# Kernel optimization log

Hardware: AMD Instinct MI355X
Metric: run time of the kernel (lower is better)

## Reference

```python
import jax, jax.numpy as jnp
import numpy as np
import math

TWO_PI = 2.0 * math.pi
LN_EPS = 1e-5


def _phase(pos_f, d):
    # periods[i, j] = i * d + j + 2 ; phi[s, i, j] = cos(2*pi*k_s / periods[i, j])
    i = jnp.arange(d, dtype=jnp.float32)
    periods = i[:, None] * d + i[None, :] + 2.0  # (d, d)
    return jnp.cos(TWO_PI * pos_f[:, None, None] / periods)  # (S, d, d)


def _layernorm(x, g, b):
    mu = jnp.mean(x, axis=-1, keepdims=True)
    var = jnp.mean(jnp.square(x - mu), axis=-1, keepdims=True)
    return (x - mu) * jax.lax.rsqrt(var + LN_EPS) * g + b


def _pos_nk(x, P, phi):
    # Nk[b, s, i] = sum_j P[i, j] * x[b, s, j] * phi[s, i, j]
    return jnp.einsum('bsj,ij,sij->bsi', x, P, phi)


def setup_inputs() -> dict:
    key = jax.random.key(0)
    ks = jax.random.split(key, 10)
    B, S, V, D = 4, 4096, 64, 128
    NTOK = 64  # 4^3 k-mer tokens
    u = lambda k, shp, a: jax.random.uniform(k, shp, jnp.float32, -a, a)
    return {
        'tokens': jax.random.randint(ks[0], (B, S), 0, NTOK, dtype=jnp.int32),
        'positions': jnp.arange(S, dtype=jnp.int32),
        'emb': jax.random.normal(ks[1], (NTOK, V), jnp.float32),
        'char_P': u(ks[2], (V, V), 0.1),
        'M1': u(ks[3], (D, V), 0.5),
        'P1': u(ks[4], (D, D), 0.1),
        'g1': jnp.ones((D,), jnp.float32),
        'b1': jnp.zeros((D,), jnp.float32),
        'R1': u(ks[5], (D, V), 0.1),
        'M2': u(ks[6], (D, D), 0.5),
        'P2': u(ks[7], (D, D), 0.1),
        'g2': jnp.ones((D,), jnp.float32),
        'b2': jnp.zeros((D,), jnp.float32),
    }


def reference(tokens, positions, emb, char_P, M1, P1, g1, b1, R1, M2, P2, g2, b2):
    pos_f = positions.astype(jnp.float32)
    V, D1, D2 = emb.shape[1], M1.shape[0], M2.shape[0]
    # char level (Layer 0): embedding + position-modulated mixing
    x = emb[tokens]                               # (B, S, V)
    h = _pos_nk(x, char_P, _phase(pos_f, V))      # (B, S, V)
    # Layer 1: separate residual (in_dim != out_dim -> linear proj)
    t1 = jnp.einsum('bsj,ij->bsi', h, M1)         # (B, S, D1)
    n1 = _pos_nk(_layernorm(t1, g1, b1), P1, _phase(pos_f, D1))
    h1 = n1 + jnp.einsum('bsj,ij->bsi', h, R1)
    # Layer 2: shared residual (residual = x @ M.T, pre-norm)
    t2 = jnp.einsum('bsj,ij->bsi', h1, M2)        # (B, S, D2)
    n2 = _pos_nk(_layernorm(t2, g2, b2), P2, _phase(pos_f, D2))
    return n2 + t2
```

## Files before the change

kernel.cpp:

```cpp
#include <hip/hip_runtime.h>

typedef unsigned short u16;
typedef unsigned int   u32;

#define BB 4
#define SS 4096
#define VV 64
#define DD 128

#define CPT_OFF 0
#define M1T_OFF 4096
#define R1T_OFF 12288
#define P1T_OFF 20480
#define M2T_OFF 36864
#define P2T_OFF 53248
#define EMB_OFF 69632
#define G1_OFF  73728
#define B1_OFF  73856
#define G2_OFF  73984
#define B2_OFF  74112
#define WS_F32_WEIGHTS 74240

__device__ __forceinline__ float bf2f(u16 u) {
    return __uint_as_float(((u32)u) << 16);
}
__device__ __forceinline__ float ldany(const void* p, int idx, bool f32) {
    return f32 ? ((const float*)p)[idx] : bf2f(((const u16*)p)[idx]);
}
__device__ __forceinline__ float phase_cos(float pos, float pf) {
    float x = pos * __builtin_amdgcn_rcpf(pf);
    float r = x - floorf(x);
    return __builtin_amdgcn_cosf(r);
}
__device__ __forceinline__ u32 pk_bf16(float lo, float hi) {
    u32 a = __float_as_uint(lo) + 0x8000u;
    u32 b = __float_as_uint(hi) + 0x8000u;
    return __builtin_amdgcn_perm(b, a, 0x07060302u);
}
__device__ __forceinline__ float bfhalf(u32 word, int hi) {
    return __uint_as_float(hi ? (word & 0xffff0000u) : (word << 16));
}
__device__ __forceinline__ float f4get(float4 v, int i) {
    return i == 0 ? v.x : i == 1 ? v.y : i == 2 ? v.z : v.w;
}
__device__ __forceinline__ float4 f4sum(float4 a, float4 b) {
    return make_float4(a.x + b.x, a.y + b.y, a.z + b.z, a.w + b.w);
}
__device__ __forceinline__ float4 fma4(float s, float4 v, float4 a) {
    return make_float4(fmaf(s, v.x, a.x), fmaf(s, v.y, a.y),
                       fmaf(s, v.z, a.z), fmaf(s, v.w, a.w));
}

__global__ void prep_ws(const void* __restrict__ cP,  const void* __restrict__ M1,
                        const void* __restrict__ R1,  const void* __restrict__ P1,
                        const void* __restrict__ M2,  const void* __restrict__ P2,
                        const void* __restrict__ emb, const void* __restrict__ g1,
                        const void* __restrict__ b1,  const void* __restrict__ g2,
                        const void* __restrict__ b2,  float* __restrict__ wsf)
{
    const bool f32 = (((const u32*)g1)[0] == 0x3F800000u);
    const int m = blockIdx.x;
    const int t = threadIdx.x;
    if (m == 17) {
        for (int idx = t; idx < 4608; idx += 256) {
            float v; int dst;
            if (idx < 4096) { v = ldany(emb, idx, f32); dst = EMB_OFF + idx; }
            else {
                int off = idx - 4096, which = off >> 7, e = off & 127;
                const void* p = (which == 0) ? g1 : (which == 1) ? b1
                              : (which == 2) ? g2 : b2;
                v = ldany(p, e, f32);
                dst = G1_OFF + which * 128 + e;
            }
            wsf[dst] = v;
        }
        return;
    }
    __shared__ float tile[64][65];
    const void* src; int doff, R, C, ti0, tj0;
    if (m == 0)      { src = cP; doff = CPT_OFF; R = 64;  C = 64;  ti0 = 0;            tj0 = 0; }
    else if (m <= 2) { src = M1; doff = M1T_OFF; R = 128; C = 64;  ti0 = (m - 1) * 64; tj0 = 0; }
    else if (m <= 4) { src = R1; doff = R1T_OFF; R = 128; C = 64;  ti0 = (m - 3) * 64; tj0 = 0; }
    else {
        const int k = m - 5, w = k >> 2, q = k & 3;
        src  = (w == 0) ? P1 : (w == 1) ? M2 : P2;
        doff = (w == 0) ? P1T_OFF : (w == 1) ? M2T_OFF : P2T_OFF;
        R = 128; C = 128; ti0 = (q >> 1) * 64; tj0 = (q & 1) * 64;
    }
    float* dst = wsf + doff;
    #pragma unroll
    for (int k = 0; k < 16; ++k) {
        int idx = k * 256 + t;
        int i = idx >> 6, j = idx & 63;
        tile[i][j] = ldany(src, (ti0 + i) * C + (tj0 + j), f32);
    }
    __syncthreads();
    #pragma unroll
    for (int k = 0; k < 16; ++k) {
        int idx = k * 256 + t;
        int j = idx >> 6, i = idx & 63;
        int gj = tj0 + j, gi = ti0 + i;
        dst[((gj >> 2) * R + gi) * 4 + (gj & 3)] = tile[i][j];
    }
}

template<bool WS>
__global__ void __launch_bounds__(256, 4)
fused_hier(const int* __restrict__ tokens,
           const int* __restrict__ positions,
           const void* __restrict__ emb,
           const void* __restrict__ cP,
           const void* __restrict__ M1,
           const void* __restrict__ P1,
           const void* __restrict__ g1,
           const void* __restrict__ b1,
           const void* __restrict__ R1,
           const void* __restrict__ M2,
           const void* __restrict__ P2,
           const void* __restrict__ g2,
           const void* __restrict__ b2,
           const float* __restrict__ wsf,
           float* __restrict__ out)
{
    __shared__ float4 x4v[VV];
    __shared__ float4 h4v[VV];
    __shared__ float4 lnv[DD];
    __shared__ float4 h1v[DD];
    __shared__ float4 t2v[DD];
    __shared__ float4 t14v[DD];
    __shared__ float4 partv[512];

    float* lnf = (float*)lnv;

    const int t = threadIdx.x;
    const int s = blockIdx.x;
    if (s >= SS) return;
    const bool f32 = WS ? true : (((const u32*)g1)[0] == 0x3F800000u);
    const float pos = (float)positions[s];
    const int i6 = t & 63,  q4 = t >> 6;
    const int i7 = t & 127, h2 = t >> 7;
    const int w  = t >> 6,  l  = t & 63;

    if (t < 64) {
        int tk0 = tokens[0 * SS + s], tk1 = tokens[1 * SS + s];
        int tk2 = tokens[2 * SS + s], tk3 = tokens[3 * SS + s];
        float4 xb;
        xb.x = WS ? wsf[EMB_OFF + tk0 * VV + i6] : ldany(emb, tk0 * VV + i6, f32);
        xb.y = WS ? wsf[EMB_OFF + tk1 * VV + i6] : ldany(emb, tk1 * VV + i6, f32);
        xb.z = WS ? wsf[EMB_OFF + tk2 * VV + i6] : ldany(emb, tk2 * VV + i6, f32);
        xb.w = WS ? wsf[EMB_OFF + tk3 * VV + i6] : ldany(emb, tk3 * VV + i6, f32);
        x4v[i6] = xb;
    }
    __syncthreads();

    {
        float4 a = make_float4(0, 0, 0, 0);
        const int jb = q4 * 16;
        float pf = (float)(i6 * VV + jb + 2);
        #pragma unroll
        for (int q = 0; q < 4; ++q) {
            const int jg = q4 * 4 + q;
            float4 w4;
            if (WS) w4 = *(const float4*)&wsf[CPT_OFF + (jg * VV + i6) * 4];
            #pragma unroll
            for (int k = 0; k < 4; ++k) {
                const int j = jb + q * 4 + k;
                float c  = phase_cos(pos, pf);
                float wt = (WS ? f4get(w4, k) : ldany(cP, i6 * VV + j, f32)) * c;
                a = fma4(wt, x4v[j], a);
                pf += 1.0f;
            }
        }
        partv[q4 * 64 + i6] = a;
    }
    __syncthreads();

    if (t < 64) {
        h4v[i6] = f4sum(f4sum(partv[i6], partv[64 + i6]),
                        f4sum(partv[128 + i6], partv[192 + i6]));
    }
    __syncthreads();

    {
        float4 at = make_float4(0, 0, 0, 0), ar = make_float4(0, 0, 0, 0);
        #pragma unroll
        for (int q = 0; q < 8; ++q) {
            const int jg = h2 * 8 + q;
            float4 m4, r4;
            if (WS) {
                m4 = *(const float4*)&wsf[M1T_OFF + (jg * DD + i7) * 4];
                r4 = *(const float4*)&wsf[R1T_OFF + (jg * DD + i7) * 4];
            }
            #pragma unroll
            for (int k = 0; k < 4; ++k) {
                const int j = h2 * 32 + q * 4 + k;
                float mv = WS ? f4get(m4, k) : ldany(M1, i7 * VV + j, f32);
                float rv = WS ? f4get(r4, k) : ldany(R1, i7 * VV + j, f32);
                float4 hb = h4v[j];
                at = fma4(mv, hb, at);
                ar = fma4(rv, hb, ar);
            }
        }
        partv[h2 * 128 + i7]       = at;
        partv[256 + h2 * 128 + i7] = ar;
    }
    __syncthreads();

    if (t < 128) {
        t14v[i7] = f4sum(partv[i7], partv[128 + i7]);
        h1v[i7]  = f4sum(partv[256 + i7], partv[384 + i7]);
    }
    __syncthreads();

    {
        float v0 = f4get(t14v[l], w), v1 = f4get(t14v[l + 64], w);
        float s1 = v0 + v1;
        #pragma unroll
        for (int m = 1; m < 64; m <<= 1) s1 += __shfl_xor(s1, m, 64);
        float mu = s1 * (1.0f / 128.0f);
        float d0 = v0 - mu, d1 = v1 - mu;
        float s2 = d0 * d0 + d1 * d1;
        #pragma unroll
        for (int m = 1; m < 64; m <<= 1) s2 += __shfl_xor(s2, m, 64);
        float rs = rsqrtf(s2 * (1.0f / 128.0f) + 1e-5f);
        float ga = WS ? wsf[G1_OFF + l]      : ldany(g1, l, f32);
        float gb = WS ? wsf[G1_OFF + l + 64] : ldany(g1, l + 64, f32);
        float ba = WS ? wsf[B1_OFF + l]      : ldany(b1, l, f32);
        float bb = WS ? wsf[B1_OFF + l + 64] : ldany(b1, l + 64, f32);
        lnf[l * 4 + w]        = d0 * rs * ga + ba;
        lnf[(l + 64) * 4 + w] = d1 * rs * gb + bb;
    }
    __syncthreads();

    u32 phc[32];
    {
        float4 acc = make_float4(0, 0, 0, 0);
        float pf = (float)(i7 * DD + h2 * 64 + 2);
        float cprev = 0.f;
        #pragma unroll
        for (int o = 0; o < 8; ++o) {
            float4 wa, wb;
            if (WS) {
                wa = *(const float4*)&wsf[P1T_OFF + ((h2 * 16 + 2 * o    ) * DD + i7) * 4];
                wb = *(const float4*)&wsf[P1T_OFF + ((h2 * 16 + 2 * o + 1) * DD + i7) * 4];
            }
            #pragma unroll
            for (int e = 0; e < 8; ++e) {
                const int j = h2 * 64 + o * 8 + e;
                float c = phase_cos(pos, pf);
                pf += 1.0f;
                if ((e & 1) == 0) cprev = c;
                else phc[o * 4 + (e >> 1)] = pk_bf16(cprev, c);
                float wv = WS ? (e < 4 ? f4get(wa, e) : f4get(wb, e - 4))
                              : ldany(P1, i7 * DD + j, f32);
                acc = fma4(wv * c, lnv[j], acc);
            }
        }
        partv[h2 * 128 + i7] = acc;
    }
    __syncthreads();

    if (t < 128) {
        h1v[i7] = f4sum(h1v[i7], f4sum(partv[i7], partv[128 + i7]));
    }
    __syncthreads();

    {
        float4 acc = make_float4(0, 0, 0, 0);
        #pragma unroll
        for (int q = 0; q < 16; ++q) {
            const int jg = h2 * 16 + q;
            float4 m4;
            if (WS) m4 = *(const float4*)&wsf[M2T_OFF + (jg * DD + i7) * 4];
            #pragma unroll
            for (int k = 0; k < 4; ++k) {
                const int j = h2 * 64 + q * 4 + k;
                float mv = WS ? f4get(m4, k) : ldany(M2, i7 * DD + j, f32);
                acc = fma4(mv, h1v[j], acc);
            }
        }
        partv[h2 * 128 + i7] = acc;
    }
    __syncthreads();

    if (t < 128) {
        t2v[i7] = f4sum(partv[i7], partv[128 + i7]);
    }
    __syncthreads();

    {
        float v0 = f4get(t2v[l], w), v1 = f4get(t2v[l + 64], w);
        float s1 = v0 + v1;
        #pragma unroll
        for (int m = 1; m < 64; m <<= 1) s1 += __shfl_xor(s1, m, 64);
        float mu = s1 * (1.0f / 128.0f);
        float d0 = v0 - mu, d1 = v1 - mu;
        float s2 = d0 * d0 + d1 * d1;
        #pragma unroll
        for (int m = 1; m < 64; m <<= 1) s2 += __shfl_xor(s2, m, 64);
        float rs = rsqrtf(s2 * (1.0f / 128.0f) + 1e-5f);
        float ga = WS ? wsf[G2_OFF + l]      : ldany(g2, l, f32);
        float gb = WS ? wsf[G2_OFF + l + 64] : ldany(g2, l + 64, f32);
        float ba = WS ? wsf[B2_OFF + l]      : ldany(b2, l, f32);
        float bb = WS ? wsf[B2_OFF + l + 64] : ldany(b2, l + 64, f32);
        lnf[l * 4 + w]        = d0 * rs * ga + ba;
        lnf[(l + 64) * 4 + w] = d1 * rs * gb + bb;
    }
    __syncthreads();

    {
        float4 acc = make_float4(0, 0, 0, 0);
        #pragma unroll
        for (int o = 0; o < 8; ++o) {
            float4 wa, wb;
            if (WS) {
                wa = *(const float4*)&wsf[P2T_OFF + ((h2 * 16 + 2 * o    ) * DD + i7) * 4];
                wb = *(const float4*)&wsf[P2T_OFF + ((h2 * 16 + 2 * o + 1) * DD + i7) * 4];
            }
            #pragma unroll
            for (int e = 0; e < 8; ++e) {
                const int j = h2 * 64 + o * 8 + e;
                float c = bfhalf(phc[o * 4 + (e >> 1)], e & 1);
                float wv = WS ? (e < 4 ? f4get(wa, e) : f4get(wb, e - 4))
                              : ldany(P2, i7 * DD + j, f32);
                acc = fma4(wv * c, lnv[j], acc);
            }
        }
        partv[h2 * 128 + i7] = acc;
    }
    __syncthreads();

    if (t < 128) {
        float4 n2 = f4sum(partv[i7], partv[128 + i7]);
        float4 o4 = f4sum(n2, t2v[i7]);
        out[(0 * SS + s) * DD + i7] = o4.x;
        out[(1 * SS + s) * DD + i7] = o4.y;
        out[(2 * SS + s) * DD + i7] = o4.z;
        out[(3 * SS + s) * DD + i7] = o4.w;
    }
}

extern "C" void kernel_launch(void* const* d_in, const int* in_sizes, int n_in,
                              void* d_out, int out_size, void* d_ws, size_t ws_size,
                              hipStream_t stream)
{
    const int* tokens    = (const int*)d_in[0];
    const int* positions = (const int*)d_in[1];
    const void* emb = d_in[2];
    const void* cP  = d_in[3];
    const void* M1  = d_in[4];
    const void* P1  = d_in[5];
    const void* g1  = d_in[6];
    const void* b1  = d_in[7];
    const void* R1  = d_in[8];
    const void* M2  = d_in[9];
    const void* P2  = d_in[10];
    const void* g2  = d_in[11];
    const void* b2  = d_in[12];
    float* out = (float*)d_out;
    float* wsf = (float*)d_ws;

    const bool tw = (ws_size >= (size_t)WS_F32_WEIGHTS * sizeof(float));
    if (tw) {
        prep_ws<<<18, 256, 0, stream>>>(cP, M1, R1, P1, M2, P2, emb,
                                        g1, b1, g2, b2, wsf);
        fused_hier<true><<<SS, 256, 0, stream>>>(tokens, positions, emb, cP, M1, P1,
                                                 g1, b1, R1, M2, P2, g2, b2, wsf, out);
    } else {
        fused_hier<false><<<SS, 256, 0, stream>>>(tokens, positions, emb, cP, M1, P1,
                                                  g1, b1, R1, M2, P2, g2, b2, wsf, out);
    }
}
```

Before: 151.9 us.

## Spread reductions across all threads and recompute layer-2 phases instead of caching

Partial-sum buffers become batch-major scalar arrays, so every stage's cross-half reduction runs on all 256 threads instead of a 64- or 128-thread subset. The embedding gather is split the same way, and the layer-1 residual is kept in registers. The bf16-packed phase cache (phc) carried from layer 1 to layer 2 is dropped, and cosines are recomputed in layer 2 in full fp32. This frees 32 registers and removes bf16 rounding, at the cost of twice as many transcendental evaluations.

```diff
diff --git a/kernel.cpp b/kernel.cpp
--- a/kernel.cpp
+++ b/kernel.cpp
@@ -32,19 +32,8 @@
     float r = x - floorf(x);
     return __builtin_amdgcn_cosf(r);
 }
-__device__ __forceinline__ u32 pk_bf16(float lo, float hi) {
-    u32 a = __float_as_uint(lo) + 0x8000u;
-    u32 b = __float_as_uint(hi) + 0x8000u;
-    return __builtin_amdgcn_perm(b, a, 0x07060302u);
-}
-__device__ __forceinline__ float bfhalf(u32 word, int hi) {
-    return __uint_as_float(hi ? (word & 0xffff0000u) : (word << 16));
-}
 __device__ __forceinline__ float f4get(float4 v, int i) {
     return i == 0 ? v.x : i == 1 ? v.y : i == 2 ? v.z : v.w;
-}
-__device__ __forceinline__ float4 f4sum(float4 a, float4 b) {
-    return make_float4(a.x + b.x, a.y + b.y, a.z + b.z, a.w + b.w);
 }
 __device__ __forceinline__ float4 fma4(float s, float4 v, float4 a) {
     return make_float4(fmaf(s, v.x, a.x), fmaf(s, v.y, a.y),
@@ -126,11 +115,14 @@
     __shared__ float4 h4v[VV];
     __shared__ float4 lnv[DD];
     __shared__ float4 h1v[DD];
-    __shared__ float4 t2v[DD];
-    __shared__ float4 t14v[DD];
-    __shared__ float4 partv[512];
-
+    __shared__ float  t14p[4 * DD];
+    __shared__ float  t2p[4 * DD];
+    __shared__ float  partp[2048];
+
+    float* x4  = (float*)x4v;
+    float* h4  = (float*)h4v;
     float* lnf = (float*)lnv;
+    float* h1f = (float*)h1v;
 
     const int t = threadIdx.x;
     const int s = blockIdx.x;
@@ -141,15 +133,10 @@
     const int i7 = t & 127, h2 = t >> 7;
     const int w  = t >> 6,  l  = t & 63;
 
-    if (t < 64) {
-        int tk0 = tokens[0 * SS + s], tk1 = tokens[1 * SS + s];
-        int tk2 = tokens[2 * SS + s], tk3 = tokens[3 * SS + s];
-        float4 xb;
-        xb.x = WS ? wsf[EMB_OFF + tk0 * VV + i6] : ldany(emb, tk0 * VV + i6, f32);
-        xb.y = WS ? wsf[EMB_OFF + tk1 * VV + i6] : ldany(emb, tk1 * VV + i6, f32);
-        xb.z = WS ? wsf[EMB_OFF + tk2 * VV + i6] : ldany(emb, tk2 * VV + i6, f32);
-        xb.w = WS ? wsf[EMB_OFF + tk3 * VV + i6] : ldany(emb, tk3 * VV + i6, f32);
-        x4v[i6] = xb;
+    {
+        int tok = tokens[q4 * SS + s];
+        float v = WS ? wsf[EMB_OFF + tok * VV + i6] : ldany(emb, tok * VV + i6, f32);
+        x4[i6 * 4 + q4] = v;
     }
     __syncthreads();
 
@@ -171,13 +158,16 @@
                 pf += 1.0f;
             }
         }
-        partv[q4 * 64 + i6] = a;
-    }
-    __syncthreads();
-
-    if (t < 64) {
-        h4v[i6] = f4sum(f4sum(partv[i6], partv[64 + i6]),
-                        f4sum(partv[128 + i6], partv[192 + i6]));
+        #pragma unroll
+        for (int b = 0; b < 4; ++b)
+            partp[b * 256 + q4 * 64 + i6] = f4get(a, b);
+    }
+    __syncthreads();
+
+    {
+        float hv = partp[q4 * 256 + i6]       + partp[q4 * 256 + 64 + i6]
+                 + partp[q4 * 256 + 128 + i6] + partp[q4 * 256 + 192 + i6];
+        h4[i6 * 4 + q4] = hv;
     }
     __syncthreads();
 
@@ -201,19 +191,26 @@
                 ar = fma4(rv, hb, ar);
             }
         }
-        partv[h2 * 128 + i7]       = at;
-        partv[256 + h2 * 128 + i7] = ar;
-    }
-    __syncthreads();
-
-    if (t < 128) {
-        t14v[i7] = f4sum(partv[i7], partv[128 + i7]);
-        h1v[i7]  = f4sum(partv[256 + i7], partv[384 + i7]);
-    }
-    __syncthreads();
-
-    {
-        float v0 = f4get(t14v[l], w), v1 = f4get(t14v[l + 64], w);
+        #pragma unroll
+        for (int b = 0; b < 4; ++b) {
+            partp[b * 256 + h2 * 128 + i7]        = f4get(at, b);
+            partp[1024 + b * 256 + h2 * 128 + i7] = f4get(ar, b);
+        }
+    }
+    __syncthreads();
+
+    float res0, res1;
+    {
+        const int b0 = h2 * 2, b1 = b0 + 1;
+        t14p[b0 * 128 + i7] = partp[b0 * 256 + i7] + partp[b0 * 256 + 128 + i7];
+        t14p[b1 * 128 + i7] = partp[b1 * 256 + i7] + partp[b1 * 256 + 128 + i7];
+        res0 = partp[1024 + b0 * 256 + i7] + partp[1024 + b0 * 256 + 128 + i7];
+        res1 = partp[1024 + b1 * 256 + i7] + partp[1024 + b1 * 256 + 128 + i7];
+    }
+    __syncthreads();
+
+    {
+        float v0 = t14p[w * 128 + l], v1 = t14p[w * 128 + 64 + l];
         float s1 = v0 + v1;
         #pragma unroll
         for (int m = 1; m < 64; m <<= 1) s1 += __shfl_xor(s1, m, 64);
@@ -232,36 +229,33 @@
     }
     __syncthreads();
 
-    u32 phc[32];
     {
         float4 acc = make_float4(0, 0, 0, 0);
         float pf = (float)(i7 * DD + h2 * 64 + 2);
-        float cprev = 0.f;
-        #pragma unroll
-        for (int o = 0; o < 8; ++o) {
-            float4 wa, wb;
-            if (WS) {
-                wa = *(const float4*)&wsf[P1T_OFF + ((h2 * 16 + 2 * o    ) * DD + i7) * 4];
-                wb = *(const float4*)&wsf[P1T_OFF + ((h2 * 16 + 2 * o + 1) * DD + i7) * 4];
-            }
-            #pragma unroll
-            for (int e = 0; e < 8; ++e) {
-                const int j = h2 * 64 + o * 8 + e;
+        #pragma unroll
+        for (int q = 0; q < 16; ++q) {
+            const int jg = h2 * 16 + q;
+            float4 w4;
+            if (WS) w4 = *(const float4*)&wsf[P1T_OFF + (jg * DD + i7) * 4];
+            #pragma unroll
+            for (int k = 0; k < 4; ++k) {
+                const int j = h2 * 64 + q * 4 + k;
                 float c = phase_cos(pos, pf);
+                float wt = (WS ? f4get(w4, k) : ldany(P1, i7 * DD + j, f32)) * c;
+                acc = fma4(wt, lnv[j], acc);
                 pf += 1.0f;
-                if ((e & 1) == 0) cprev = c;
-                else phc[o * 4 + (e >> 1)] = pk_bf16(cprev, c);
-                float wv = WS ? (e < 4 ? f4get(wa, e) : f4get(wb, e - 4))
-                              : ldany(P1, i7 * DD + j, f32);
-                acc = fma4(wv * c, lnv[j], acc);
-            }
-        }
-        partv[h2 * 128 + i7] = acc;
-    }
-    __syncthreads();
-
-    if (t < 128) {
-        h1v[i7] = f4sum(h1v[i7], f4sum(partv[i7], partv[128 + i7]));
+            }
+        }
+        #pragma unroll
+        for (int b = 0; b < 4; ++b)
+            partp[b * 256 + h2 * 128 + i7] = f4get(acc, b);
+    }
+    __syncthreads();
+
+    {
+        const int b0 = h2 * 2, b1 = b0 + 1;
+        h1f[i7 * 4 + b0] = res0 + partp[b0 * 256 + i7] + partp[b0 * 256 + 128 + i7];
+        h1f[i7 * 4 + b1] = res1 + partp[b1 * 256 + i7] + partp[b1 * 256 + 128 + i7];
     }
     __syncthreads();
 
@@ -279,17 +273,21 @@
                 acc = fma4(mv, h1v[j], acc);
             }
         }
-        partv[h2 * 128 + i7] = acc;
-    }
-    __syncthreads();
-
-    if (t < 128) {
-        t2v[i7] = f4sum(partv[i7], partv[128 + i7]);
-    }
-    __syncthreads();
-
-    {
-        float v0 = f4get(t2v[l], w), v1 = f4get(t2v[l + 64], w);
+        #pragma unroll
+        for (int b = 0; b < 4; ++b)
+            partp[b * 256 + h2 * 128 + i7] = f4get(acc, b);
+    }
+    __syncthreads();
+
+    {
+        const int b0 = h2 * 2, b1 = b0 + 1;
+        t2p[b0 * 128 + i7] = partp[b0 * 256 + i7] + partp[b0 * 256 + 128 + i7];
+        t2p[b1 * 128 + i7] = partp[b1 * 256 + i7] + partp[b1 * 256 + 128 + i7];
+    }
+    __syncthreads();
+
+    {
+        float v0 = t2p[w * 128 + l], v1 = t2p[w * 128 + 64 + l];
         float s1 = v0 + v1;
         #pragma unroll
         for (int m = 1; m < 64; m <<= 1) s1 += __shfl_xor(s1, m, 64);
@@ -310,33 +308,33 @@
 
     {
         float4 acc = make_float4(0, 0, 0, 0);
-        #pragma unroll
-        for (int o = 0; o < 8; ++o) {
-            float4 wa, wb;
-            if (WS) {
-                wa = *(const float4*)&wsf[P2T_OFF + ((h2 * 16 + 2 * o    ) * DD + i7) * 4];
-                wb = *(const float4*)&wsf[P2T_OFF + ((h2 * 16 + 2 * o + 1) * DD + i7) * 4];
-            }
-            #pragma unroll
-            for (int e = 0; e < 8; ++e) {
-                const int j = h2 * 64 + o * 8 + e;
-                float c = bfhalf(phc[o * 4 + (e >> 1)], e & 1);
-                float wv = WS ? (e < 4 ? f4get(wa, e) : f4get(wb, e - 4))
-                              : ldany(P2, i7 * DD + j, f32);
-                acc = fma4(wv * c, lnv[j], acc);
-            }
-        }
-        partv[h2 * 128 + i7] = acc;
-    }
-    __syncthreads();
-
-    if (t < 128) {
-        float4 n2 = f4sum(partv[i7], partv[128 + i7]);
-        float4 o4 = f4sum(n2, t2v[i7]);
-        out[(0 * SS + s) * DD + i7] = o4.x;
-        out[(1 * SS + s) * DD + i7] = o4.y;
-        out[(2 * SS + s) * DD + i7] = o4.z;
-        out[(3 * SS + s) * DD + i7] = o4.w;
+        float pf = (float)(i7 * DD + h2 * 64 + 2);
+        #pragma unroll
+        for (int q = 0; q < 16; ++q) {
+            const int jg = h2 * 16 + q;
+            float4 w4;
+            if (WS) w4 = *(const float4*)&wsf[P2T_OFF + (jg * DD + i7) * 4];
+            #pragma unroll
+            for (int k = 0; k < 4; ++k) {
+                const int j = h2 * 64 + q * 4 + k;
+                float c = phase_cos(pos, pf);
+                float wt = (WS ? f4get(w4, k) : ldany(P2, i7 * DD + j, f32)) * c;
+                acc = fma4(wt, lnv[j], acc);
+                pf += 1.0f;
+            }
+        }
+        #pragma unroll
+        for (int b = 0; b < 4; ++b)
+            partp[b * 256 + h2 * 128 + i7] = f4get(acc, b);
+    }
+    __syncthreads();
+
+    {
+        const int b0 = h2 * 2, b1 = b0 + 1;
+        float v0 = partp[b0 * 256 + i7] + partp[b0 * 256 + 128 + i7] + t2p[b0 * 128 + i7];
+        float v1 = partp[b1 * 256 + i7] + partp[b1 * 256 + 128 + i7] + t2p[b1 * 128 + i7];
+        out[(b0 * SS + s) * DD + i7] = v0;
+        out[(b1 * SS + s) * DD + i7] = v1;
     }
 }
 
```

After: 149.5 us. Within noise of the previous version (-1.6%).
